# Kernel optimization log

Measured on AMD Instinct MI355X. Metric: run time of the kernel, lower is better.

## Reference

```python
import jax, jax.numpy as jnp
import numpy as np

B, N, D = 4, 512, 256  # batch, num_diseases, feature_dim == hidden_dim
H = 256                # hidden_dim
EPS = 1e-5

def _layernorm(x, g, b):
    m = jnp.mean(x, axis=-1, keepdims=True)
    v = jnp.mean((x - m) ** 2, axis=-1, keepdims=True)
    return (x - m) * jax.lax.rsqrt(v + EPS) * g + b

def setup_inputs() -> dict:
    key = jax.random.key(0)
    ks = jax.random.split(key, 16)
    s = 0.02
    return {
        "x": jax.random.normal(ks[0], (B, N, D), jnp.float32),
        "area_matrix": jax.random.uniform(ks[1], (B, N), jnp.float32),
        "co_occurrence": jax.random.uniform(ks[2], (N, N), jnp.float32),
        "Wq": jax.random.normal(ks[3], (H, D), jnp.float32) * s,
        "bq": jnp.zeros((H,), jnp.float32),
        "Wk": jax.random.normal(ks[4], (H, D), jnp.float32) * s,
        "bk": jnp.zeros((H,), jnp.float32),
        "Wv": jax.random.normal(ks[5], (H, D), jnp.float32) * s,
        "bv": jnp.zeros((H,), jnp.float32),
        "We1": jax.random.normal(ks[6], (H, 2), jnp.float32) * 0.5,
        "be1": jnp.zeros((H,), jnp.float32),
        "We2": jax.random.normal(ks[7], (1, H), jnp.float32) * s,
        "be2": jnp.zeros((1,), jnp.float32),
        "Wo": jax.random.normal(ks[8], (H, H), jnp.float32) * s,
        "bo": jnp.zeros((H,), jnp.float32),
        "g_ot": jnp.ones((H,), jnp.float32),
        "b_ot": jnp.zeros((H,), jnp.float32),
        "g1": jnp.ones((H,), jnp.float32),
        "b1": jnp.zeros((H,), jnp.float32),
        "g2": jnp.ones((H,), jnp.float32),
        "b2": jnp.zeros((H,), jnp.float32),
    }

def reference(x, area_matrix, co_occurrence, Wq, bq, Wk, bk, Wv, bv,
              We1, be1, We2, be2, Wo, bo, g_ot, b_ot, g1, b1, g2, b2):
    # projections: (B, N, H)
    q = jnp.einsum('bnd,hd->bnh', x, Wq) + bq
    k = jnp.einsum('bnd,hd->bnh', x, Wk) + bk
    v = jnp.einsum('bnd,hd->bnh', x, Wv) + bv
    attn_scores = jnp.einsum('bih,bjh->bij', q, k) / jnp.sqrt(jnp.float32(H))
    # edge inputs: (B, N, N, 2) = stack(broadcast area along last N, broadcast co-occ along batch)
    area = jnp.broadcast_to(area_matrix[:, :, None], (B, N, N))
    co = jnp.broadcast_to(co_occurrence[None], (B, N, N))
    edge_inputs = jnp.stack([area, co], axis=-1)
    h = jax.nn.relu(jnp.einsum('bije,he->bijh', edge_inputs, We1) + be1)
    edge_weights = jax.nn.sigmoid(jnp.einsum('bijh,oh->bijo', h, We2) + be2)[..., 0]
    attn_probs = jax.nn.softmax(attn_scores * edge_weights, axis=-1)  # dropout = identity (eval)
    out = jnp.einsum('bij,bjh->bih', attn_probs, v)
    out = _layernorm(out, g1, b1)
    out = jax.nn.relu(_layernorm(jnp.einsum('bnh,oh->bno', out, Wo) + bo, g_ot, b_ot))
    out = _layernorm(out + x, g2, b2)
    return out
```

## Files before the change

### kernel.cpp

```cpp
#include <hip/hip_runtime.h>

typedef unsigned short u16;
typedef unsigned int u32;

#define NB 4
#define NN 512
#define ND 256
#define NH 256
#define TI 4

typedef __attribute__((ext_vector_type(8))) short short8;
typedef __attribute__((ext_vector_type(4))) float f32x4;

__device__ __forceinline__ u16 bfq(float f) {
    u32 t; __builtin_memcpy(&t, &f, 4);
    u32 r = (t + 0x7FFFu + ((t >> 16) & 1u)) >> 16;
    return (u16)r;
}

__device__ __forceinline__ float waveReduceSum(float v) {
#pragma unroll
    for (int o = 32; o > 0; o >>= 1) v += __shfl_down(v, o);
    return v;
}

__device__ __forceinline__ void blockReduce8(float4& va, float4& vb, float4* red) {
#pragma unroll
    for (int o = 32; o > 0; o >>= 1) {
        va.x += __shfl_down(va.x, o); va.y += __shfl_down(va.y, o);
        va.z += __shfl_down(va.z, o); va.w += __shfl_down(va.w, o);
        vb.x += __shfl_down(vb.x, o); vb.y += __shfl_down(vb.y, o);
        vb.z += __shfl_down(vb.z, o); vb.w += __shfl_down(vb.w, o);
    }
    int wid = threadIdx.x >> 6;
    __syncthreads();
    if ((threadIdx.x & 63) == 0) { red[2 * wid] = va; red[2 * wid + 1] = vb; }
    __syncthreads();
    float4 ra = red[0], rb = red[1];
#pragma unroll
    for (int w = 1; w < 8; ++w) {
        float4 ua = red[2 * w], ub = red[2 * w + 1];
        ra.x += ua.x; ra.y += ua.y; ra.z += ua.z; ra.w += ua.w;
        rb.x += ub.x; rb.y += ub.y; rb.z += ub.z; rb.w += ub.w;
    }
    va = ra; vb = rb;
}

__global__ __launch_bounds__(256) void prep_kernel(
    const float* __restrict__ x, const float* __restrict__ Wq,
    const float* __restrict__ Wk, const float* __restrict__ Wv,
    const float* __restrict__ Wo,
    u16* __restrict__ xb, u16* __restrict__ wb)
{
    const int idx4 = (blockIdx.x * 256 + threadIdx.x) * 4;
    const float* src;
    u16* dst;
    int off;
    if (idx4 < 524288) { src = x; dst = xb; off = idx4; }
    else {
        int u = idx4 - 524288;
        int which = u >> 16; off = u & 65535;
        src = (which == 0) ? Wq : (which == 1) ? Wk : (which == 2) ? Wv : Wo;
        dst = wb + which * 65536;
    }
    float4 f = *(const float4*)(src + off);
    u32 lo = (u32)bfq(f.x) | ((u32)bfq(f.y) << 16);
    u32 hi = (u32)bfq(f.z) | ((u32)bfq(f.w) << 16);
    *(uint2*)(dst + off) = make_uint2(lo, hi);
}

__global__ __launch_bounds__(256) void qkv_mfma(
    const u16* __restrict__ xb, const u16* __restrict__ wb,
    const float* __restrict__ bq, const float* __restrict__ bk, const float* __restrict__ bv,
    u16* __restrict__ qb, u16* __restrict__ kb, u16* __restrict__ vt)
{
    const int lane = threadIdx.x & 63, wave = threadIdx.x >> 6;
    const int r0 = blockIdx.x * 64 + wave * 16;
    const int out0 = blockIdx.y * 16;
    const int which = blockIdx.y >> 4;
    const float* bia = (which == 0) ? bq : (which == 1) ? bk : bv;

    const int m = lane & 15, koff = (lane >> 4) * 8;
    const u16* Ap = xb + (size_t)(r0 + m) * 256 + koff;
    const u16* Bp = wb + which * 65536 + (size_t)((out0 & 255) + m) * 256 + koff;

    f32x4 acc = {0.f, 0.f, 0.f, 0.f};
#pragma unroll
    for (int ks = 0; ks < 8; ++ks) {
        short8 a  = *(const short8*)(Ap + ks * 32);
        short8 bb = *(const short8*)(Bp + ks * 32);
        acc = __builtin_amdgcn_mfma_f32_16x16x32_bf16(a, bb, acc, 0, 0, 0);
    }

    const int oc = (out0 + m) & 255;
    const float bias = bia[oc];
    const int rbase = r0 + (lane >> 4) * 4;
#pragma unroll
    for (int reg = 0; reg < 4; ++reg) {
        int R = rbase + reg;
        u16 val = bfq(acc[reg] + bias);
        if (which == 0)      qb[(size_t)R * 256 + oc] = val;
        else if (which == 1) kb[(size_t)R * 256 + oc] = val;
        else                 vt[((size_t)(R >> 9) * 256 + oc) * 512 + (R & 511)] = val;
    }
}

__global__ __launch_bounds__(256) void s_gemm(
    const u16* __restrict__ qb, const u16* __restrict__ kb, float* __restrict__ S)
{
    const int lane = threadIdx.x & 63, wave = threadIdx.x >> 6;
    const int job = blockIdx.x * 4 + wave;
    const int b = job >> 10, rem = job & 1023;
    const int i0 = (rem >> 5) * 16, j0 = (rem & 31) * 16;
    const int m = lane & 15, koff = (lane >> 4) * 8;
    const u16* Ap = qb + (size_t)(b * 512 + i0 + m) * 256 + koff;
    const u16* Bp = kb + (size_t)(b * 512 + j0 + m) * 256 + koff;

    f32x4 acc = {0.f, 0.f, 0.f, 0.f};
#pragma unroll
    for (int ks = 0; ks < 8; ++ks) {
        short8 a   = *(const short8*)(Ap + ks * 32);
        short8 bb  = *(const short8*)(Bp + ks * 32);
        acc = __builtin_amdgcn_mfma_f32_16x16x32_bf16(a, bb, acc, 0, 0, 0);
    }
    const int col = j0 + m;
    const int rbase = i0 + (lane >> 4) * 4;
#pragma unroll
    for (int reg = 0; reg < 4; ++reg)
        S[(size_t)(b * 512 + rbase + reg) * 512 + col] = acc[reg];
}

#define PSTR 520
#define YSTR 264
__global__ __launch_bounds__(512) void fused_kernel(
    const float* __restrict__ x, const float* __restrict__ area, const float* __restrict__ co,
    const float* __restrict__ We1, const float* __restrict__ be1,
    const float* __restrict__ We2, const float* __restrict__ be2,
    const u16* __restrict__ wob, const float* __restrict__ bo,
    const float* __restrict__ g_ot, const float* __restrict__ b_ot,
    const float* __restrict__ g1, const float* __restrict__ b1,
    const float* __restrict__ g2, const float* __restrict__ b2,
    const float* __restrict__ S, const u16* __restrict__ vt,
    float* __restrict__ out)
{
    const int tid = threadIdx.x;
    const int b = blockIdx.x >> 7;
    const int i0 = (blockIdx.x & 127) << 2;
    const int lane = tid & 63, w = tid >> 6;

    __shared__ float histS[1024], histB[1024];
    __shared__ float pvbuf[1024];
    __shared__ u16 srow16[16 * PSTR];
    __shared__ u16 y16[16 * YSTR];
    __shared__ float4 red8b[16];
    __shared__ float sBaseS[4], sBaseB[4], redA[8], redB[8];

    const float be2f = be2[0];

    histS[tid] = 0.f; histS[tid + 512] = 0.f;
    histB[tid] = 0.f; histB[tid + 512] = 0.f;
    {
        u32* s32 = (u32*)srow16;
        for (int i = tid; i < 4160; i += 512) s32[i] = 0u;
        u32* y32 = (u32*)y16;
        for (int i = tid; i < 2112; i += 512) y32[i] = 0u;
    }
    __syncthreads();

    {
        const int s = tid >> 7, h0 = tid & 127;
        const float a = area[b * NN + i0 + s];
        float baS = 0.f, baB = 0.f;
#pragma unroll
        for (int k = 0; k < 2; ++k) {
            const int h = h0 + 128 * k;
            const float w10 = We1[2 * h], w11 = We1[2 * h + 1];
            const float w2v = We2[h], be1v = be1[h];
            const float al = fmaf(a, w10, be1v);
            const float sl = w11 * w2v, bb = al * w2v;
            if (w11 == 0.f) {
                if (al > 0.f) baB += bb;
            } else {
                float tt = -al / w11;
                if (w11 > 0.f) {
                    if (tt <= 0.f)      { baS += sl; baB += bb; }
                    else if (tt < 1.f) {
                        int u = (int)(tt * 256.f); u = u > 255 ? 255 : u;
                        atomicAdd(&histS[s * 256 + u], sl);
                        atomicAdd(&histB[s * 256 + u], bb);
                    }
                } else {
                    if (tt >= 1.f)      { baS += sl; baB += bb; }
                    else if (tt > 0.f) {
                        baS += sl; baB += bb;
                        int u = (int)(tt * 256.f); u = u > 255 ? 255 : u;
                        atomicAdd(&histS[s * 256 + u], -sl);
                        atomicAdd(&histB[s * 256 + u], -bb);
                    }
                }
            }
        }
        float rS = waveReduceSum(baS), rB = waveReduceSum(baB);
        if (lane == 0) { redA[w] = rS; redB[w] = rB; }
    }
    __syncthreads();
    if (tid < 4) {
        sBaseS[tid] = redA[2 * tid] + redA[2 * tid + 1];
        sBaseB[tid] = redB[2 * tid] + redB[2 * tid + 1];
    }

    {
        const int s = w & 3;
        float* hp = (w < 4) ? histS : histB;
        float b0 = hp[s * 256 + 4 * lane + 0];
        float b1 = hp[s * 256 + 4 * lane + 1];
        float b2 = hp[s * 256 + 4 * lane + 2];
        float b3 = hp[s * 256 + 4 * lane + 3];
        float p0 = b0, p1 = p0 + b1, p2 = p1 + b2, p3 = p2 + b3;
        float incl = p3;
#pragma unroll
        for (int off = 1; off < 64; off <<= 1) {
            float t = __shfl_up(incl, off);
            if (lane >= off) incl += t;
        }
        float excl = incl - p3;
        hp[s * 256 + 4 * lane + 0] = p0 + excl;
        hp[s * 256 + 4 * lane + 1] = p1 + excl;
        hp[s * 256 + 4 * lane + 2] = p2 + excl;
        hp[s * 256 + 4 * lane + 3] = p3 + excl;
    }
    __syncthreads();

    {
        const float* Sp = S + (size_t)(b * NN + i0) * 512 + tid;
#pragma unroll
        for (int ti = 0; ti < TI; ++ti) {
            float c = co[(size_t)(i0 + ti) * NN + tid];
            int u = (int)(c * 256.f); u = u > 255 ? 255 : u;
            float Sg = sBaseS[ti] + histS[ti * 256 + u];
            float Bg = sBaseB[ti] + histB[ti * 256 + u];
            float e = fmaf(c, Sg, Bg) + be2f;
            float ew = 1.f / (1.f + __expf(-e));
            srow16[ti * PSTR + tid] = bfq(__expf(Sp[(size_t)ti * 512] * 0.0625f * ew));
        }
        __syncthreads();
    }

    {
        const int m = lane & 15, koff = (lane >> 4) * 8;
        const int t0 = 2 * w, t1 = 2 * w + 1;
        const u16* B0p = vt + ((size_t)(b * 256 + t0 * 16 + m)) * 512 + koff;
        const u16* B1p = vt + ((size_t)(b * 256 + t1 * 16 + m)) * 512 + koff;
        const u16* Arow = srow16 + m * PSTR + koff;
        f32x4 acc0 = {0.f, 0.f, 0.f, 0.f}, acc1 = {0.f, 0.f, 0.f, 0.f};
#pragma unroll
        for (int ks = 0; ks < 16; ++ks) {
            short8 a  = *(const short8*)(Arow + ks * 32);
            short8 b0 = *(const short8*)(B0p + ks * 32);
            short8 b1 = *(const short8*)(B1p + ks * 32);
            acc0 = __builtin_amdgcn_mfma_f32_16x16x32_bf16(a, b0, acc0, 0, 0, 0);
            acc1 = __builtin_amdgcn_mfma_f32_16x16x32_bf16(a, b1, acc1, 0, 0, 0);
        }
        __syncthreads();
        if (lane < 16) {
#pragma unroll
            for (int reg = 0; reg < 4; ++reg) {
                pvbuf[reg * 256 + t0 * 16 + lane] = acc0[reg];
                pvbuf[reg * 256 + t1 * 16 + lane] = acc1[reg];
            }
        }
        __syncthreads();
    }

    const int hP = tid & 255, half = tid >> 8;
    float4 sa, sb;
    float accv[TI];
#pragma unroll
    for (int ti = 0; ti < TI; ++ti) {
        accv[ti] = (half == 0) ? pvbuf[ti * 256 + hP] : 0.f;
        ((float*)&sa)[ti] = accv[ti];
        ((float*)&sb)[ti] = accv[ti] * accv[ti];
    }
    blockReduce8(sa, sb, red8b);
    if (half == 0) {
        const float g1v = g1[hP], b1v = b1[hP];
#pragma unroll
        for (int ti = 0; ti < TI; ++ti) {
            float mean = ((const float*)&sa)[ti] * (1.f / 256.f);
            float var = fmaxf(((const float*)&sb)[ti] * (1.f / 256.f) - mean * mean, 0.f);
            y16[ti * YSTR + hP] = bfq((accv[ti] - mean) * rsqrtf(var + 1e-5f) * g1v + b1v);
        }
    }
    __syncthreads();

    {
        const int m = lane & 15, koff = (lane >> 4) * 8;
        const int t0 = 2 * w, t1 = 2 * w + 1;
        const u16* B0p = wob + (size_t)(t0 * 16 + m) * 256 + koff;
        const u16* B1p = wob + (size_t)(t1 * 16 + m) * 256 + koff;
        const u16* Arow = y16 + m * YSTR + koff;
        f32x4 acc0 = {0.f, 0.f, 0.f, 0.f}, acc1 = {0.f, 0.f, 0.f, 0.f};
#pragma unroll
        for (int ks = 0; ks < 8; ++ks) {
            short8 a  = *(const short8*)(Arow + ks * 32);
            short8 b0 = *(const short8*)(B0p + ks * 32);
            short8 b1 = *(const short8*)(B1p + ks * 32);
            acc0 = __builtin_amdgcn_mfma_f32_16x16x32_bf16(a, b0, acc0, 0, 0, 0);
            acc1 = __builtin_amdgcn_mfma_f32_16x16x32_bf16(a, b1, acc1, 0, 0, 0);
        }
        __syncthreads();
        if (lane < 16) {
#pragma unroll
            for (int reg = 0; reg < 4; ++reg) {
                pvbuf[reg * 256 + t0 * 16 + lane] = acc0[reg];
                pvbuf[reg * 256 + t1 * 16 + lane] = acc1[reg];
            }
        }
        __syncthreads();
    }

    float acc2[TI];
    {
        const float bov = (half == 0) ? bo[hP] : 0.f;
#pragma unroll
        for (int ti = 0; ti < TI; ++ti) {
            acc2[ti] = (half == 0) ? pvbuf[ti * 256 + hP] + bov : 0.f;
            ((float*)&sa)[ti] = acc2[ti];
            ((float*)&sb)[ti] = acc2[ti] * acc2[ti];
        }
    }
    blockReduce8(sa, sb, red8b);
    float z[TI];
    const float gotv = (half == 0) ? g_ot[hP] : 0.f;
    const float botv = (half == 0) ? b_ot[hP] : 0.f;
#pragma unroll
    for (int ti = 0; ti < TI; ++ti) {
        float mean = ((const float*)&sa)[ti] * (1.f / 256.f);
        float var = fmaxf(((const float*)&sb)[ti] * (1.f / 256.f) - mean * mean, 0.f);
        z[ti] = fmaxf((acc2[ti] - mean) * rsqrtf(var + 1e-5f) * gotv + botv, 0.f);
    }

    float tt[TI];
#pragma unroll
    for (int ti = 0; ti < TI; ++ti) {
        tt[ti] = (half == 0) ? z[ti] + x[(size_t)(b * NN + i0 + ti) * ND + hP] : 0.f;
        ((float*)&sa)[ti] = tt[ti]; ((float*)&sb)[ti] = tt[ti] * tt[ti];
    }
    blockReduce8(sa, sb, red8b);
    if (half == 0) {
        const float g2v = g2[hP], b2v = b2[hP];
#pragma unroll
        for (int ti = 0; ti < TI; ++ti) {
            float mean = ((const float*)&sa)[ti] * (1.f / 256.f);
            float var = fmaxf(((const float*)&sb)[ti] * (1.f / 256.f) - mean * mean, 0.f);
            float o = (tt[ti] - mean) * rsqrtf(var + 1e-5f) * g2v + b2v;
            out[(size_t)(b * NN + i0 + ti) * NH + hP] = o;
        }
    }
}

extern "C" void kernel_launch(void* const* d_in, const int* in_sizes, int n_in,
                              void* d_out, int out_size, void* d_ws, size_t ws_size,
                              hipStream_t stream) {
    const float* x    = (const float*)d_in[0];
    const float* area = (const float*)d_in[1];
    const float* co   = (const float*)d_in[2];
    const float* Wq   = (const float*)d_in[3];
    const float* bq   = (const float*)d_in[4];
    const float* Wk   = (const float*)d_in[5];
    const float* bk   = (const float*)d_in[6];
    const float* Wv   = (const float*)d_in[7];
    const float* bv   = (const float*)d_in[8];
    const float* We1  = (const float*)d_in[9];
    const float* be1  = (const float*)d_in[10];
    const float* We2  = (const float*)d_in[11];
    const float* be2  = (const float*)d_in[12];
    const float* Wo   = (const float*)d_in[13];
    const float* bo   = (const float*)d_in[14];
    const float* g_ot = (const float*)d_in[15];
    const float* b_ot = (const float*)d_in[16];
    const float* g1   = (const float*)d_in[17];
    const float* b1   = (const float*)d_in[18];
    const float* g2   = (const float*)d_in[19];
    const float* b2   = (const float*)d_in[20];

    u16*  xb  = (u16*)d_ws;
    u16*  wb  = xb + (size_t)2048 * 256;
    u16*  qb  = wb + (size_t)4 * 65536;
    u16*  kb  = qb + (size_t)2048 * 256;
    u16*  vt  = kb + (size_t)2048 * 256;
    float* S  = (float*)(vt + (size_t)2048 * 256);

    prep_kernel<<<768, 256, 0, stream>>>(x, Wq, Wk, Wv, Wo, xb, wb);
    qkv_mfma<<<dim3(32, 48), 256, 0, stream>>>(xb, wb, bq, bk, bv, qb, kb, vt);
    s_gemm<<<1024, 256, 0, stream>>>(qb, kb, S);
    fused_kernel<<<NB * NN / TI, 512, 0, stream>>>(x, area, co, We1, be1, We2, be2,
                                                   wb + 3 * 65536, bo,
                                                   g_ot, b_ot, g1, b1, g2, b2,
                                                   S, vt, (float*)d_out);
}
```

Measured before the change: 155.7 us.

## Fuse QK^T score GEMM into the fused attention kernel

Removes the separate s_gemm kernel and the global score buffer. Each fused block loads its 4 query rows into shared memory and computes its score rows against K with MFMA, keeping them in shared memory. This removes a kernel launch and a round trip of the full score matrix through global memory. In exchange, each block reads all of K for its batch and wastes MFMA rows, since only 4 of 16 tile rows are valid.

New measurement: 161.8 us. 1.04x slower.

```diff
diff --git a/kernel.cpp b/kernel.cpp
--- a/kernel.cpp
+++ b/kernel.cpp
@@ -105,31 +105,6 @@
     }
 }
 
-__global__ __launch_bounds__(256) void s_gemm(
-    const u16* __restrict__ qb, const u16* __restrict__ kb, float* __restrict__ S)
-{
-    const int lane = threadIdx.x & 63, wave = threadIdx.x >> 6;
-    const int job = blockIdx.x * 4 + wave;
-    const int b = job >> 10, rem = job & 1023;
-    const int i0 = (rem >> 5) * 16, j0 = (rem & 31) * 16;
-    const int m = lane & 15, koff = (lane >> 4) * 8;
-    const u16* Ap = qb + (size_t)(b * 512 + i0 + m) * 256 + koff;
-    const u16* Bp = kb + (size_t)(b * 512 + j0 + m) * 256 + koff;
-
-    f32x4 acc = {0.f, 0.f, 0.f, 0.f};
-#pragma unroll
-    for (int ks = 0; ks < 8; ++ks) {
-        short8 a   = *(const short8*)(Ap + ks * 32);
-        short8 bb  = *(const short8*)(Bp + ks * 32);
-        acc = __builtin_amdgcn_mfma_f32_16x16x32_bf16(a, bb, acc, 0, 0, 0);
-    }
-    const int col = j0 + m;
-    const int rbase = i0 + (lane >> 4) * 4;
-#pragma unroll
-    for (int reg = 0; reg < 4; ++reg)
-        S[(size_t)(b * 512 + rbase + reg) * 512 + col] = acc[reg];
-}
-
 #define PSTR 520
 #define YSTR 264
 __global__ __launch_bounds__(512) void fused_kernel(
@@ -140,7 +115,7 @@
     const float* __restrict__ g_ot, const float* __restrict__ b_ot,
     const float* __restrict__ g1, const float* __restrict__ b1,
     const float* __restrict__ g2, const float* __restrict__ b2,
-    const float* __restrict__ S, const u16* __restrict__ vt,
+    const u16* __restrict__ qb, const u16* __restrict__ kb, const u16* __restrict__ vt,
     float* __restrict__ out)
 {
     const int tid = threadIdx.x;
@@ -150,6 +125,7 @@
 
     __shared__ float histS[1024], histB[1024];
     __shared__ float pvbuf[1024];
+    __shared__ float sblock[4 * 512];
     __shared__ u16 srow16[16 * PSTR];
     __shared__ u16 y16[16 * YSTR];
     __shared__ float4 red8b[16];
@@ -168,6 +144,10 @@
     __syncthreads();
 
     {
+        const u32* qsrc = (const u32*)(qb + (size_t)(b * NN + i0) * 256);
+        const int ti = tid >> 7, idx = tid & 127;
+        ((u32*)(y16 + ti * YSTR))[idx] = qsrc[ti * 128 + idx];
+
         const int s = tid >> 7, h0 = tid & 127;
         const float a = area[b * NN + i0 + s];
         float baS = 0.f, baB = 0.f;
@@ -229,10 +209,33 @@
         hp[s * 256 + 4 * lane + 2] = p2 + excl;
         hp[s * 256 + 4 * lane + 3] = p3 + excl;
     }
-    __syncthreads();
-
-    {
-        const float* Sp = S + (size_t)(b * NN + i0) * 512 + tid;
+
+    {
+        const int m = lane & 15, koff = (lane >> 4) * 8;
+        const u16* Arow = y16 + m * YSTR + koff;
+        short8 afr[8];
+#pragma unroll
+        for (int ks = 0; ks < 8; ++ks) afr[ks] = *(const short8*)(Arow + ks * 32);
+#pragma unroll
+        for (int t = 0; t < 4; ++t) {
+            const int j0 = (w + 8 * t) * 16;
+            const u16* Bp = kb + (size_t)(b * 512 + j0 + m) * 256 + koff;
+            f32x4 acc = {0.f, 0.f, 0.f, 0.f};
+#pragma unroll
+            for (int ks = 0; ks < 8; ++ks) {
+                short8 bb = *(const short8*)(Bp + ks * 32);
+                acc = __builtin_amdgcn_mfma_f32_16x16x32_bf16(afr[ks], bb, acc, 0, 0, 0);
+            }
+            if (lane < 16) {
+#pragma unroll
+                for (int reg = 0; reg < 4; ++reg)
+                    sblock[reg * 512 + j0 + lane] = acc[reg];
+            }
+        }
+    }
+    __syncthreads();
+
+    {
 #pragma unroll
         for (int ti = 0; ti < TI; ++ti) {
             float c = co[(size_t)(i0 + ti) * NN + tid];
@@ -241,7 +244,7 @@
             float Bg = sBaseB[ti] + histB[ti * 256 + u];
             float e = fmaf(c, Sg, Bg) + be2f;
             float ew = 1.f / (1.f + __expf(-e));
-            srow16[ti * PSTR + tid] = bfq(__expf(Sp[(size_t)ti * 512] * 0.0625f * ew));
+            srow16[ti * PSTR + tid] = bfq(__expf(sblock[ti * 512 + tid] * 0.0625f * ew));
         }
         __syncthreads();
     }
@@ -261,7 +264,6 @@
             acc0 = __builtin_amdgcn_mfma_f32_16x16x32_bf16(a, b0, acc0, 0, 0, 0);
             acc1 = __builtin_amdgcn_mfma_f32_16x16x32_bf16(a, b1, acc1, 0, 0, 0);
         }
-        __syncthreads();
         if (lane < 16) {
 #pragma unroll
             for (int reg = 0; reg < 4; ++reg) {
@@ -389,13 +391,11 @@
     u16*  qb  = wb + (size_t)4 * 65536;
     u16*  kb  = qb + (size_t)2048 * 256;
     u16*  vt  = kb + (size_t)2048 * 256;
-    float* S  = (float*)(vt + (size_t)2048 * 256);
 
     prep_kernel<<<768, 256, 0, stream>>>(x, Wq, Wk, Wv, Wo, xb, wb);
     qkv_mfma<<<dim3(32, 48), 256, 0, stream>>>(xb, wb, bq, bk, bv, qb, kb, vt);
-    s_gemm<<<1024, 256, 0, stream>>>(qb, kb, S);
     fused_kernel<<<NB * NN / TI, 512, 0, stream>>>(x, area, co, We1, be1, We2, be2,
                                                    wb + 3 * 65536, bo,
                                                    g_ot, b_ot, g1, b1, g2, b2,
-                                                   S, vt, (float*)d_out);
-}
+                                                   qb, kb, vt, (float*)d_out);
+}
```
